# Kernel tuning notes

Measured on AMD Instinct MI355X. Metric: run time of the kernel, lower is better.

## Reference

```python
import jax, jax.numpy as jnp
import numpy as np

NUM_NODES = 100000
NUM_EDGES = 600000
NUM_GRAPHS = 1000
EMB = 128


def setup_inputs() -> dict:
    key = jax.random.key(0)
    ks = jax.random.split(key, 12)
    x = jax.random.normal(ks[0], (NUM_NODES, 4), dtype=jnp.float32)
    edge_index = jax.random.randint(ks[1], (2, NUM_EDGES), 0, NUM_NODES, dtype=jnp.int32)
    x_scalar = jax.random.normal(ks[2], (NUM_GRAPHS, 4), dtype=jnp.float32)
    batch_index = jnp.sort(jax.random.randint(ks[3], (NUM_NODES,), 0, NUM_GRAPHS, dtype=jnp.int32))
    def glorot(k, shape):
        fan_in, fan_out = shape[0], shape[1]
        s = jnp.sqrt(2.0 / (fan_in + fan_out)).astype(jnp.float32)
        return jax.random.normal(k, shape, dtype=jnp.float32) * s
    return {
        "x": x,
        "edge_index": edge_index,
        "x_scalar": x_scalar,
        "batch_index": batch_index,
        "W0": glorot(ks[4], (4, EMB)), "b0": jnp.zeros((EMB,), jnp.float32),
        "W1": glorot(ks[5], (EMB, EMB)), "b1": jnp.zeros((EMB,), jnp.float32),
        "W2": glorot(ks[6], (EMB, EMB)), "b2": jnp.zeros((EMB,), jnp.float32),
        "W3": glorot(ks[7], (EMB, EMB)), "b3": jnp.zeros((EMB,), jnp.float32),
        "Wl1": glorot(ks[8], (EMB + 4, 64)), "bl1": jnp.zeros((64,), jnp.float32),
        "Wl2": glorot(ks[9], (64, 1)), "bl2": jnp.zeros((1,), jnp.float32),
    }


def _gcn_norm(edge_index, num_nodes):
    # PyG GCNConv default: add self-loops, symmetric normalization
    loop = jnp.arange(num_nodes, dtype=edge_index.dtype)
    src = jnp.concatenate([edge_index[0], loop])
    dst = jnp.concatenate([edge_index[1], loop])
    deg = jax.ops.segment_sum(jnp.ones_like(src, dtype=jnp.float32), dst,
                              num_segments=num_nodes)
    dinv = jnp.where(deg > 0, jax.lax.rsqrt(jnp.maximum(deg, 1e-12)), 0.0)
    norm = dinv[src] * dinv[dst]  # [E+N]
    return src, dst, norm


def _gcn_conv(h, src, dst, norm, W, b, num_nodes):
    h = h @ W                                   # [N, out]
    msg = h[src] * norm[:, None]                # gather + normalize
    out = jax.ops.segment_sum(msg, dst, num_segments=num_nodes)  # scatter-add
    return out + b


def reference(x, edge_index, x_scalar, batch_index,
              W0, b0, W1, b1, W2, b2, W3, b3, Wl1, bl1, Wl2, bl2):
    n = x.shape[0]
    src, dst, norm = _gcn_norm(edge_index, n)
    h = jax.nn.relu(_gcn_conv(x, src, dst, norm, W0, b0, n))
    h = jax.nn.relu(_gcn_conv(h, src, dst, norm, W1, b1, n))
    h = jax.nn.relu(_gcn_conv(h, src, dst, norm, W2, b2, n))
    h = jax.nn.relu(_gcn_conv(h, src, dst, norm, W3, b3, n))
    # global mean pool over batch_index
    sums = jax.ops.segment_sum(h, batch_index, num_segments=NUM_GRAPHS)
    cnts = jax.ops.segment_sum(jnp.ones((n,), jnp.float32), batch_index,
                               num_segments=NUM_GRAPHS)
    pooled = sums / jnp.maximum(cnts, 1.0)[:, None]          # [G, EMB]
    feat = jnp.concatenate([pooled, x_scalar], axis=1)       # [G, EMB+4]
    out = jax.nn.relu(feat @ Wl1 + bl1) @ Wl2 + bl2          # [G, 1]
    return out
```

## Files before the change

kernel.cpp:

```cpp
#include <hip/hip_runtime.h>

#define NN 100000
#define EE 600000
#define GG 1000
#define NB ((NN + 255) / 256)
#define CAP 32
#define LDSPAD 136

typedef __bf16 bf16x8 __attribute__((ext_vector_type(8)));
typedef float f32x4 __attribute__((ext_vector_type(4)));
typedef unsigned int u32;

__device__ inline float2 bf2_to_f2(u32 u) {
  return make_float2(__uint_as_float(u << 16), __uint_as_float(u & 0xffff0000u));
}
__device__ inline u32 f2_to_bf2(float a, float b) {
  union { __bf16 h[2]; u32 u; } pk;
  pk.h[0] = (__bf16)a; pk.h[1] = (__bf16)b;
  return pk.u;
}


__global__ void k_init(int* cnt, int* gstart) {
  int i = blockIdx.x * 256 + threadIdx.x;
  if (i < NN) cnt[i] = 0;
  if (i <= GG) gstart[i] = NN;
}

__global__ void k_fill(const int* __restrict__ src, const int* __restrict__ dst,
                       int* cnt, int2* __restrict__ wbucket) {
  int e = blockIdx.x * 256 + threadIdx.x;
  if (e >= EE) return;
  int s = src[e], d = dst[e];
  int pos = atomicAdd(&cnt[d], 1);
  if (pos < CAP - 1) wbucket[d * CAP + pos].x = s;
}

__global__ void k_wb(const int* __restrict__ cnt, const int* __restrict__ batch,
                     int* gstart,
                     const float* __restrict__ W1, const float* __restrict__ W2,
                     const float* __restrict__ W3,
                     __bf16* __restrict__ Wt1, __bf16* __restrict__ Wt2,
                     __bf16* __restrict__ Wt3, int2* __restrict__ wbucket) {
  int gid = blockIdx.x * 256 + threadIdx.x;
  if (gid < 3 * 16384) {
    int which = gid >> 14, idx = gid & 16383;
    int n = idx >> 7, k = idx & 127;
    const float* W = (which == 0) ? W1 : (which == 1) ? W2 : W3;
    __bf16* Wt = (which == 0) ? Wt1 : (which == 1) ? Wt2 : Wt3;
    Wt[(size_t)n * 128 + k] = (__bf16)W[(size_t)k * 128 + n];
  }
  if (gid < NN) {
    int b = batch[gid];
    if (gid == 0) {
      for (int g = 0; g <= b; ++g) gstart[g] = 0;
    } else {
      int prev = batch[gid - 1];
      for (int g = prev + 1; g <= b; ++g) gstart[g] = gid;
    }
  }
  if (gid < NN * CAP) {
    int d = gid >> 5, slot = gid & 31;
    int m = min(cnt[d], CAP - 1);
    int mp = (m + 4) & ~3;
    if (slot < mp) {
      float dd = rsqrtf((float)(cnt[d] + 1));
      int s; float w;
      if (slot < m)      { s = wbucket[gid].x; w = rsqrtf((float)(cnt[s] + 1)) * dd; }
      else if (slot == m){ s = d;              w = dd * dd; }
      else               { s = d;              w = 0.f; }
      wbucket[gid] = make_int2(s, __float_as_int(w));
    }
  }
}

__global__ void k_l0(const float4* __restrict__ x, const int* __restrict__ cnt,
                     const int2* __restrict__ wbucket,
                     const float* __restrict__ W0, const float* __restrict__ b0,
                     u32* __restrict__ hout2) {
  int gid = blockIdx.x * 256 + threadIdx.x;
  if (gid >= NN * 16) return;
  int node = gid >> 4, cg = gid & 15;
  int m1 = min(cnt[node], CAP - 1) + 1;
  float4 yv = make_float4(0.f, 0.f, 0.f, 0.f);
  for (int e = 0; e < m1; ++e) {
    int2 md = wbucket[(size_t)node * CAP + e];
    float wgt = __int_as_float(md.y);
    float4 v = x[md.x];
    yv.x = fmaf(wgt, v.x, yv.x);
    yv.y = fmaf(wgt, v.y, yv.y);
    yv.z = fmaf(wgt, v.z, yv.z);
    yv.w = fmaf(wgt, v.w, yv.w);
  }
  float v[8];
  #pragma unroll
  for (int k = 0; k < 2; ++k) {
    float4 b = *(const float4*)(b0 + cg * 8 + k * 4);
    v[k * 4 + 0] = b.x; v[k * 4 + 1] = b.y; v[k * 4 + 2] = b.z; v[k * 4 + 3] = b.w;
  }
  #pragma unroll
  for (int k = 0; k < 4; ++k) {
    float yk = (k == 0) ? yv.x : (k == 1) ? yv.y : (k == 2) ? yv.z : yv.w;
    float4 wa = *(const float4*)(W0 + k * 128 + cg * 8);
    float4 wb = *(const float4*)(W0 + k * 128 + cg * 8 + 4);
    v[0] = fmaf(yk, wa.x, v[0]); v[1] = fmaf(yk, wa.y, v[1]);
    v[2] = fmaf(yk, wa.z, v[2]); v[3] = fmaf(yk, wa.w, v[3]);
    v[4] = fmaf(yk, wb.x, v[4]); v[5] = fmaf(yk, wb.y, v[5]);
    v[6] = fmaf(yk, wb.z, v[6]); v[7] = fmaf(yk, wb.w, v[7]);
  }
  uint4 o;
  o.x = f2_to_bf2(fmaxf(v[0], 0.f), fmaxf(v[1], 0.f));
  o.y = f2_to_bf2(fmaxf(v[2], 0.f), fmaxf(v[3], 0.f));
  o.z = f2_to_bf2(fmaxf(v[4], 0.f), fmaxf(v[5], 0.f));
  o.w = f2_to_bf2(fmaxf(v[6], 0.f), fmaxf(v[7], 0.f));
  *(uint4*)(hout2 + (size_t)node * 64 + cg * 4) = o;
}

__global__ __launch_bounds__(256) void k_agg23(const __bf16* __restrict__ hlin,
                                               const int* __restrict__ cnt,
                                               const int2* __restrict__ wbucket,
                                               u32* __restrict__ hout2) {
  int wid = (blockIdx.x * 4) + (threadIdx.x >> 6);
  int lane = threadIdx.x & 63;
  int ln = lane & 15, quad = lane >> 4;
  int na = wid * 2, nb = wid * 2 + 1;
  if (na >= NN) return;

  int mpa = (min(cnt[na], CAP - 1) + 4) & ~3;
  int mpb = (nb < NN) ? ((min(cnt[nb], CAP - 1) + 4) & ~3) : 0;
  int mpmin = min(mpa, mpb);

  int nodeL = (lane < 32) ? na : nb;
  int slot = lane & 31;
  int mymp = (lane < 32) ? mpa : mpb;
  int2 me = make_int2(0, 0);
  if (slot < mymp) me = wbucket[(size_t)nodeL * CAP + slot];
  int s_l = me.x, w_l = me.y;

  float aa[8] = {0.f, 0.f, 0.f, 0.f, 0.f, 0.f, 0.f, 0.f};
  float ab[8] = {0.f, 0.f, 0.f, 0.f, 0.f, 0.f, 0.f, 0.f};

  int j = 0;
  for (; j + 8 <= mpmin; j += 8) {
    int p0 = (j + quad) * 4, p1 = (j + 4 + quad) * 4;
    int sa0 = __builtin_amdgcn_ds_bpermute(p0, s_l);
    int sa1 = __builtin_amdgcn_ds_bpermute(p1, s_l);
    int sb0 = __builtin_amdgcn_ds_bpermute(128 + p0, s_l);
    int sb1 = __builtin_amdgcn_ds_bpermute(128 + p1, s_l);
    float wa0 = __int_as_float(__builtin_amdgcn_ds_bpermute(p0, w_l));
    float wa1 = __int_as_float(__builtin_amdgcn_ds_bpermute(p1, w_l));
    float wb0 = __int_as_float(__builtin_amdgcn_ds_bpermute(128 + p0, w_l));
    float wb1 = __int_as_float(__builtin_amdgcn_ds_bpermute(128 + p1, w_l));
    uint4 ua0 = *(const uint4*)(hlin + ((size_t)sa0 << 7) + ln * 8);
    uint4 ua1 = *(const uint4*)(hlin + ((size_t)sa1 << 7) + ln * 8);
    uint4 ub0 = *(const uint4*)(hlin + ((size_t)sb0 << 7) + ln * 8);
    uint4 ub1 = *(const uint4*)(hlin + ((size_t)sb1 << 7) + ln * 8);
    float2 f;
    f = bf2_to_f2(ua0.x); aa[0] = fmaf(wa0, f.x, aa[0]); aa[1] = fmaf(wa0, f.y, aa[1]);
    f = bf2_to_f2(ua0.y); aa[2] = fmaf(wa0, f.x, aa[2]); aa[3] = fmaf(wa0, f.y, aa[3]);
    f = bf2_to_f2(ua0.z); aa[4] = fmaf(wa0, f.x, aa[4]); aa[5] = fmaf(wa0, f.y, aa[5]);
    f = bf2_to_f2(ua0.w); aa[6] = fmaf(wa0, f.x, aa[6]); aa[7] = fmaf(wa0, f.y, aa[7]);
    f = bf2_to_f2(ua1.x); aa[0] = fmaf(wa1, f.x, aa[0]); aa[1] = fmaf(wa1, f.y, aa[1]);
    f = bf2_to_f2(ua1.y); aa[2] = fmaf(wa1, f.x, aa[2]); aa[3] = fmaf(wa1, f.y, aa[3]);
    f = bf2_to_f2(ua1.z); aa[4] = fmaf(wa1, f.x, aa[4]); aa[5] = fmaf(wa1, f.y, aa[5]);
    f = bf2_to_f2(ua1.w); aa[6] = fmaf(wa1, f.x, aa[6]); aa[7] = fmaf(wa1, f.y, aa[7]);
    f = bf2_to_f2(ub0.x); ab[0] = fmaf(wb0, f.x, ab[0]); ab[1] = fmaf(wb0, f.y, ab[1]);
    f = bf2_to_f2(ub0.y); ab[2] = fmaf(wb0, f.x, ab[2]); ab[3] = fmaf(wb0, f.y, ab[3]);
    f = bf2_to_f2(ub0.z); ab[4] = fmaf(wb0, f.x, ab[4]); ab[5] = fmaf(wb0, f.y, ab[5]);
    f = bf2_to_f2(ub0.w); ab[6] = fmaf(wb0, f.x, ab[6]); ab[7] = fmaf(wb0, f.y, ab[7]);
    f = bf2_to_f2(ub1.x); ab[0] = fmaf(wb1, f.x, ab[0]); ab[1] = fmaf(wb1, f.y, ab[1]);
    f = bf2_to_f2(ub1.y); ab[2] = fmaf(wb1, f.x, ab[2]); ab[3] = fmaf(wb1, f.y, ab[3]);
    f = bf2_to_f2(ub1.z); ab[4] = fmaf(wb1, f.x, ab[4]); ab[5] = fmaf(wb1, f.y, ab[5]);
    f = bf2_to_f2(ub1.w); ab[6] = fmaf(wb1, f.x, ab[6]); ab[7] = fmaf(wb1, f.y, ab[7]);
  }
  if (j < mpmin) {
    int p = (j + quad) * 4;
    int sa = __builtin_amdgcn_ds_bpermute(p, s_l);
    int sb = __builtin_amdgcn_ds_bpermute(128 + p, s_l);
    float wa = __int_as_float(__builtin_amdgcn_ds_bpermute(p, w_l));
    float wb = __int_as_float(__builtin_amdgcn_ds_bpermute(128 + p, w_l));
    uint4 ua = *(const uint4*)(hlin + ((size_t)sa << 7) + ln * 8);
    uint4 ub = *(const uint4*)(hlin + ((size_t)sb << 7) + ln * 8);
    float2 f;
    f = bf2_to_f2(ua.x); aa[0] = fmaf(wa, f.x, aa[0]); aa[1] = fmaf(wa, f.y, aa[1]);
    f = bf2_to_f2(ua.y); aa[2] = fmaf(wa, f.x, aa[2]); aa[3] = fmaf(wa, f.y, aa[3]);
    f = bf2_to_f2(ua.z); aa[4] = fmaf(wa, f.x, aa[4]); aa[5] = fmaf(wa, f.y, aa[5]);
    f = bf2_to_f2(ua.w); aa[6] = fmaf(wa, f.x, aa[6]); aa[7] = fmaf(wa, f.y, aa[7]);
    f = bf2_to_f2(ub.x); ab[0] = fmaf(wb, f.x, ab[0]); ab[1] = fmaf(wb, f.y, ab[1]);
    f = bf2_to_f2(ub.y); ab[2] = fmaf(wb, f.x, ab[2]); ab[3] = fmaf(wb, f.y, ab[3]);
    f = bf2_to_f2(ub.z); ab[4] = fmaf(wb, f.x, ab[4]); ab[5] = fmaf(wb, f.y, ab[5]);
    f = bf2_to_f2(ub.w); ab[6] = fmaf(wb, f.x, ab[6]); ab[7] = fmaf(wb, f.y, ab[7]);
    j += 4;
  }
  for (; j < mpa; j += 4) {
    int p = (j + quad) * 4;
    int s0 = __builtin_amdgcn_ds_bpermute(p, s_l);
    float w0 = __int_as_float(__builtin_amdgcn_ds_bpermute(p, w_l));
    uint4 u0 = *(const uint4*)(hlin + ((size_t)s0 << 7) + ln * 8);
    float2 f;
    f = bf2_to_f2(u0.x); aa[0] = fmaf(w0, f.x, aa[0]); aa[1] = fmaf(w0, f.y, aa[1]);
    f = bf2_to_f2(u0.y); aa[2] = fmaf(w0, f.x, aa[2]); aa[3] = fmaf(w0, f.y, aa[3]);
    f = bf2_to_f2(u0.z); aa[4] = fmaf(w0, f.x, aa[4]); aa[5] = fmaf(w0, f.y, aa[5]);
    f = bf2_to_f2(u0.w); aa[6] = fmaf(w0, f.x, aa[6]); aa[7] = fmaf(w0, f.y, aa[7]);
  }
  for (; j < mpb; j += 4) {
    int p = 128 + (j + quad) * 4;
    int s0 = __builtin_amdgcn_ds_bpermute(p, s_l);
    float w0 = __int_as_float(__builtin_amdgcn_ds_bpermute(p, w_l));
    uint4 u0 = *(const uint4*)(hlin + ((size_t)s0 << 7) + ln * 8);
    float2 f;
    f = bf2_to_f2(u0.x); ab[0] = fmaf(w0, f.x, ab[0]); ab[1] = fmaf(w0, f.y, ab[1]);
    f = bf2_to_f2(u0.y); ab[2] = fmaf(w0, f.x, ab[2]); ab[3] = fmaf(w0, f.y, ab[3]);
    f = bf2_to_f2(u0.z); ab[4] = fmaf(w0, f.x, ab[4]); ab[5] = fmaf(w0, f.y, ab[5]);
    f = bf2_to_f2(u0.w); ab[6] = fmaf(w0, f.x, ab[6]); ab[7] = fmaf(w0, f.y, ab[7]);
  }

  #pragma unroll
  for (int k = 0; k < 8; ++k) {
    aa[k] += __shfl_xor(aa[k], 16); aa[k] += __shfl_xor(aa[k], 32);
    ab[k] += __shfl_xor(ab[k], 16); ab[k] += __shfl_xor(ab[k], 32);
  }
  if (quad == 0) {
    uint4 oa;
    oa.x = f2_to_bf2(aa[0], aa[1]); oa.y = f2_to_bf2(aa[2], aa[3]);
    oa.z = f2_to_bf2(aa[4], aa[5]); oa.w = f2_to_bf2(aa[6], aa[7]);
    *(uint4*)(hout2 + (size_t)na * 64 + ln * 4) = oa;
    if (nb < NN) {
      uint4 ob;
      ob.x = f2_to_bf2(ab[0], ab[1]); ob.y = f2_to_bf2(ab[2], ab[3]);
      ob.z = f2_to_bf2(ab[4], ab[5]); ob.w = f2_to_bf2(ab[6], ab[7]);
      *(uint4*)(hout2 + (size_t)nb * 64 + ln * 4) = ob;
    }
  }
}

__global__ __launch_bounds__(256) void k_mfma(const __bf16* __restrict__ hin,
                                              const __bf16* __restrict__ Wt,
                                              const float* __restrict__ bias,
                                              __bf16* __restrict__ hout) {
  __shared__ __bf16 As[128 * LDSPAD];
  int tid = threadIdx.x;
  int row0 = blockIdx.x * 128;
  int lane = tid & 63, w = tid >> 6;
  int ln = lane & 15, quad = lane >> 4;

  bf16x8 bfrag[8][4];
  float bcol[8];
  #pragma unroll
  for (int nt = 0; nt < 8; ++nt) {
    bcol[nt] = bias[nt * 16 + ln];
    #pragma unroll
    for (int kc = 0; kc < 4; ++kc)
      bfrag[nt][kc] = *(const bf16x8*)(Wt + (size_t)(nt * 16 + ln) * 128 + kc * 32 + quad * 8);
  }

  #pragma unroll
  for (int i = 0; i < 8; ++i) {
    int eb = (i * 256 + tid) * 8;
    int r = eb >> 7, c = eb & 127;
    int gr = row0 + r;
    uint4 v = make_uint4(0, 0, 0, 0);
    if (gr < NN) v = *(const uint4*)(hin + (size_t)gr * 128 + c);
    *(uint4*)&As[r * LDSPAD + c] = v;
  }
  __syncthreads();

  f32x4 acc[2][8];
  #pragma unroll
  for (int rt = 0; rt < 2; ++rt)
    #pragma unroll
    for (int nt = 0; nt < 8; ++nt) acc[rt][nt] = (f32x4){0.f, 0.f, 0.f, 0.f};

  #pragma unroll
  for (int kc = 0; kc < 4; ++kc) {
    bf16x8 a0 = *(const bf16x8*)&As[(w * 32 + ln) * LDSPAD + kc * 32 + quad * 8];
    bf16x8 a1 = *(const bf16x8*)&As[(w * 32 + 16 + ln) * LDSPAD + kc * 32 + quad * 8];
    #pragma unroll
    for (int nt = 0; nt < 8; ++nt) {
      acc[0][nt] = __builtin_amdgcn_mfma_f32_16x16x32_bf16(a0, bfrag[nt][kc], acc[0][nt], 0, 0, 0);
      acc[1][nt] = __builtin_amdgcn_mfma_f32_16x16x32_bf16(a1, bfrag[nt][kc], acc[1][nt], 0, 0, 0);
    }
  }

  #pragma unroll
  for (int rt = 0; rt < 2; ++rt)
    #pragma unroll
    for (int nt = 0; nt < 8; ++nt)
      #pragma unroll
      for (int reg = 0; reg < 4; ++reg) {
        int gr = row0 + w * 32 + rt * 16 + quad * 4 + reg;
        if (gr < NN)
          hout[(size_t)gr * 128 + nt * 16 + ln] =
              (__bf16)fmaxf(acc[rt][nt][reg] + bcol[nt], 0.f);
      }
}

__global__ __launch_bounds__(256) void k_poolmlp(const uint2* __restrict__ h4u,
                                                 const int* __restrict__ gstart,
                                                 const float* __restrict__ xs,
                                                 const float* __restrict__ Wl1,
                                                 const float* __restrict__ bl1,
                                                 const float* __restrict__ Wl2,
                                                 const float* __restrict__ bl2,
                                                 float* __restrict__ out) {
  __shared__ float4 part[8][32];
  __shared__ float pooled[128];
  int g = blockIdx.x;
  int beg = gstart[g], end = gstart[g + 1];
  int tid = threadIdx.x;
  int cg = tid & 31;
  int rg = tid >> 5;
  float4 acc = make_float4(0.f, 0.f, 0.f, 0.f);
  for (int i = beg + rg; i < end; i += 8) {
    uint2 u = h4u[(size_t)i * 32 + cg];
    acc.x += __uint_as_float(u.x << 16);
    acc.y += __uint_as_float(u.x & 0xffff0000u);
    acc.z += __uint_as_float(u.y << 16);
    acc.w += __uint_as_float(u.y & 0xffff0000u);
  }
  part[rg][cg] = acc;
  __syncthreads();
  if (tid < 32) {
    float4 s = part[0][tid];
    #pragma unroll
    for (int r = 1; r < 8; ++r) {
      float4 v = part[r][tid];
      s.x += v.x; s.y += v.y; s.z += v.z; s.w += v.w;
    }
    float sc = 1.f / fmaxf((float)(end - beg), 1.f);
    pooled[tid * 4 + 0] = s.x * sc;
    pooled[tid * 4 + 1] = s.y * sc;
    pooled[tid * 4 + 2] = s.z * sc;
    pooled[tid * 4 + 3] = s.w * sc;
  }
  __syncthreads();
  if (tid < 64) {
    float hj = bl1[tid];
    #pragma unroll 4
    for (int k = 0; k < 128; ++k) hj = fmaf(pooled[k], Wl1[k * 64 + tid], hj);
    const float* xr = xs + g * 4;
    #pragma unroll
    for (int k = 0; k < 4; ++k) hj = fmaf(xr[k], Wl1[(128 + k) * 64 + tid], hj);
    hj = fmaxf(hj, 0.f);
    float val = hj * Wl2[tid];
    #pragma unroll
    for (int off = 32; off > 0; off >>= 1) val += __shfl_down(val, off);
    if (tid == 0) out[g] = val + bl2[0];
  }
}


extern "C" void kernel_launch(void* const* d_in, const int* in_sizes, int n_in,
                              void* d_out, int out_size, void* d_ws, size_t ws_size,
                              hipStream_t stream) {
  const float* x    = (const float*)d_in[0];
  const int*   ei   = (const int*)d_in[1];
  const float* xs   = (const float*)d_in[2];
  const int*   batch= (const int*)d_in[3];
  const float* W0   = (const float*)d_in[4];
  const float* b0   = (const float*)d_in[5];
  const float* W1   = (const float*)d_in[6];
  const float* b1   = (const float*)d_in[7];
  const float* W2   = (const float*)d_in[8];
  const float* b2   = (const float*)d_in[9];
  const float* W3   = (const float*)d_in[10];
  const float* b3   = (const float*)d_in[11];
  const float* Wl1  = (const float*)d_in[12];
  const float* bl1  = (const float*)d_in[13];
  const float* Wl2  = (const float*)d_in[14];
  const float* bl2  = (const float*)d_in[15];
  const int* srcA = ei;
  const int* dstA = ei + EE;
  float* out = (float*)d_out;

  char* p = (char*)d_ws;
  auto take = [&](size_t bytes) { char* q = p; p += (bytes + 255) & ~(size_t)255; return q; };
  __bf16* hA    = (__bf16*)take((size_t)NN * 128 * 2);
  __bf16* hB    = (__bf16*)take((size_t)NN * 128 * 2);
  int*    cnt   = (int*)take((size_t)NN * 4);
  int2*   wbucket = (int2*)take((size_t)NN * CAP * 8);
  int*    gstart= (int*)take((size_t)(GG + 1) * 4);
  __bf16* Wt1   = (__bf16*)take(16384 * 2);
  __bf16* Wt2   = (__bf16*)take(16384 * 2);
  __bf16* Wt3   = (__bf16*)take(16384 * 2);

  k_init<<<NB, 256, 0, stream>>>(cnt, gstart);
  k_fill<<<(EE + 255) / 256, 256, 0, stream>>>(srcA, dstA, cnt, wbucket);
  k_wb<<<(NN * CAP + 255) / 256, 256, 0, stream>>>(cnt, batch, gstart, W1, W2, W3,
                                                   Wt1, Wt2, Wt3, wbucket);

  k_l0<<<(NN * 16 + 255) / 256, 256, 0, stream>>>((const float4*)x, cnt, wbucket, W0, b0, (u32*)hA);
  k_agg23<<<(NN + 7) / 8, 256, 0, stream>>>(hA, cnt, wbucket, (u32*)hB);
  k_mfma<<<(NN + 127) / 128, 256, 0, stream>>>(hB, Wt1, b1, hA);
  k_agg23<<<(NN + 7) / 8, 256, 0, stream>>>(hA, cnt, wbucket, (u32*)hB);
  k_mfma<<<(NN + 127) / 128, 256, 0, stream>>>(hB, Wt2, b2, hA);
  k_agg23<<<(NN + 7) / 8, 256, 0, stream>>>(hA, cnt, wbucket, (u32*)hB);
  k_mfma<<<(NN + 127) / 128, 256, 0, stream>>>(hB, Wt3, b3, hA);

  k_poolmlp<<<GG, 256, 0, stream>>>((const uint2*)hA, gstart, xs, Wl1, bl1, Wl2, bl2, out);
}
```

Measured before the change: 349.9 us.

## Store aggregated features in MFMA fragment layout and drop LDS staging in k_mfma

The aggregation kernel now writes its output in a tiled layout of 16-node tiles that matches the MFMA operand fragment order. The GEMM kernel then loads fragments straight from global memory with no LDS staging or __syncthreads. It also swaps operand roles so each wave computes one 16-node tile and writes packed bf16 pairs per row. The aim is to remove LDS traffic and the barrier and to coalesce the input loads. The cost is reloading weight fragments from global or cache for every tile.

Result: slower. 380.2 us (+8.6%).

```diff
diff --git a/kernel.cpp b/kernel.cpp
--- a/kernel.cpp
+++ b/kernel.cpp
@@ -5,7 +5,7 @@
 #define GG 1000
 #define NB ((NN + 255) / 256)
 #define CAP 32
-#define LDSPAD 136
+#define NTILES (NN / 16)
 
 typedef __bf16 bf16x8 __attribute__((ext_vector_type(8)));
 typedef float f32x4 __attribute__((ext_vector_type(4)));
@@ -224,75 +224,51 @@
     uint4 oa;
     oa.x = f2_to_bf2(aa[0], aa[1]); oa.y = f2_to_bf2(aa[2], aa[3]);
     oa.z = f2_to_bf2(aa[4], aa[5]); oa.w = f2_to_bf2(aa[6], aa[7]);
-    *(uint4*)(hout2 + (size_t)na * 64 + ln * 4) = oa;
+    *(uint4*)(hout2 + (size_t)(na >> 4) * 1024 + ln * 64 + (na & 15) * 4) = oa;
     if (nb < NN) {
       uint4 ob;
       ob.x = f2_to_bf2(ab[0], ab[1]); ob.y = f2_to_bf2(ab[2], ab[3]);
       ob.z = f2_to_bf2(ab[4], ab[5]); ob.w = f2_to_bf2(ab[6], ab[7]);
-      *(uint4*)(hout2 + (size_t)nb * 64 + ln * 4) = ob;
-    }
-  }
-}
-
-__global__ __launch_bounds__(256) void k_mfma(const __bf16* __restrict__ hin,
+      *(uint4*)(hout2 + (size_t)(nb >> 4) * 1024 + ln * 64 + (nb & 15) * 4) = ob;
+    }
+  }
+}
+
+__global__ __launch_bounds__(256) void k_mfma(const __bf16* __restrict__ hfrag,
                                               const __bf16* __restrict__ Wt,
                                               const float* __restrict__ bias,
                                               __bf16* __restrict__ hout) {
-  __shared__ __bf16 As[128 * LDSPAD];
   int tid = threadIdx.x;
-  int row0 = blockIdx.x * 128;
   int lane = tid & 63, w = tid >> 6;
   int ln = lane & 15, quad = lane >> 4;
-
-  bf16x8 bfrag[8][4];
-  float bcol[8];
-  #pragma unroll
-  for (int nt = 0; nt < 8; ++nt) {
-    bcol[nt] = bias[nt * 16 + ln];
+  int tile = blockIdx.x * 4 + w;
+  if (tile >= NTILES) return;
+
+  f32x4 acc[8];
+  #pragma unroll
+  for (int ct = 0; ct < 8; ++ct) acc[ct] = (f32x4){0.f, 0.f, 0.f, 0.f};
+
+  const __bf16* hb = hfrag + (size_t)tile * 2048 + quad * 128 + ln * 8;
+  #pragma unroll
+  for (int kc = 0; kc < 4; ++kc) {
+    bf16x8 hf = *(const bf16x8*)(hb + kc * 512);
     #pragma unroll
-    for (int kc = 0; kc < 4; ++kc)
-      bfrag[nt][kc] = *(const bf16x8*)(Wt + (size_t)(nt * 16 + ln) * 128 + kc * 32 + quad * 8);
-  }
-
-  #pragma unroll
-  for (int i = 0; i < 8; ++i) {
-    int eb = (i * 256 + tid) * 8;
-    int r = eb >> 7, c = eb & 127;
-    int gr = row0 + r;
-    uint4 v = make_uint4(0, 0, 0, 0);
-    if (gr < NN) v = *(const uint4*)(hin + (size_t)gr * 128 + c);
-    *(uint4*)&As[r * LDSPAD + c] = v;
-  }
-  __syncthreads();
-
-  f32x4 acc[2][8];
-  #pragma unroll
-  for (int rt = 0; rt < 2; ++rt)
-    #pragma unroll
-    for (int nt = 0; nt < 8; ++nt) acc[rt][nt] = (f32x4){0.f, 0.f, 0.f, 0.f};
-
-  #pragma unroll
-  for (int kc = 0; kc < 4; ++kc) {
-    bf16x8 a0 = *(const bf16x8*)&As[(w * 32 + ln) * LDSPAD + kc * 32 + quad * 8];
-    bf16x8 a1 = *(const bf16x8*)&As[(w * 32 + 16 + ln) * LDSPAD + kc * 32 + quad * 8];
-    #pragma unroll
-    for (int nt = 0; nt < 8; ++nt) {
-      acc[0][nt] = __builtin_amdgcn_mfma_f32_16x16x32_bf16(a0, bfrag[nt][kc], acc[0][nt], 0, 0, 0);
-      acc[1][nt] = __builtin_amdgcn_mfma_f32_16x16x32_bf16(a1, bfrag[nt][kc], acc[1][nt], 0, 0, 0);
-    }
-  }
-
-  #pragma unroll
-  for (int rt = 0; rt < 2; ++rt)
-    #pragma unroll
-    for (int nt = 0; nt < 8; ++nt)
-      #pragma unroll
-      for (int reg = 0; reg < 4; ++reg) {
-        int gr = row0 + w * 32 + rt * 16 + quad * 4 + reg;
-        if (gr < NN)
-          hout[(size_t)gr * 128 + nt * 16 + ln] =
-              (__bf16)fmaxf(acc[rt][nt][reg] + bcol[nt], 0.f);
-      }
+    for (int ct = 0; ct < 8; ++ct) {
+      bf16x8 wf = *(const bf16x8*)(Wt + (size_t)(ct * 16 + ln) * 128 + kc * 32 + quad * 8);
+      acc[ct] = __builtin_amdgcn_mfma_f32_16x16x32_bf16(wf, hf, acc[ct], 0, 0, 0);
+    }
+  }
+
+  int node = tile * 16 + ln;
+  __bf16* op = hout + (size_t)node * 128 + quad * 4;
+  #pragma unroll
+  for (int ct = 0; ct < 8; ++ct) {
+    float4 bq = *(const float4*)(bias + ct * 16 + quad * 4);
+    uint2 o;
+    o.x = f2_to_bf2(fmaxf(acc[ct][0] + bq.x, 0.f), fmaxf(acc[ct][1] + bq.y, 0.f));
+    o.y = f2_to_bf2(fmaxf(acc[ct][2] + bq.z, 0.f), fmaxf(acc[ct][3] + bq.w, 0.f));
+    *(uint2*)(op + ct * 16) = o;
+  }
 }
 
 __global__ __launch_bounds__(256) void k_poolmlp(const uint2* __restrict__ h4u,
@@ -391,11 +367,11 @@
 
   k_l0<<<(NN * 16 + 255) / 256, 256, 0, stream>>>((const float4*)x, cnt, wbucket, W0, b0, (u32*)hA);
   k_agg23<<<(NN + 7) / 8, 256, 0, stream>>>(hA, cnt, wbucket, (u32*)hB);
-  k_mfma<<<(NN + 127) / 128, 256, 0, stream>>>(hB, Wt1, b1, hA);
+  k_mfma<<<(NTILES + 3) / 4, 256, 0, stream>>>(hB, Wt1, b1, hA);
   k_agg23<<<(NN + 7) / 8, 256, 0, stream>>>(hA, cnt, wbucket, (u32*)hB);
-  k_mfma<<<(NN + 127) / 128, 256, 0, stream>>>(hB, Wt2, b2, hA);
+  k_mfma<<<(NTILES + 3) / 4, 256, 0, stream>>>(hB, Wt2, b2, hA);
   k_agg23<<<(NN + 7) / 8, 256, 0, stream>>>(hA, cnt, wbucket, (u32*)hB);
-  k_mfma<<<(NN + 127) / 128, 256, 0, stream>>>(hB, Wt3, b3, hA);
+  k_mfma<<<(NTILES + 3) / 4, 256, 0, stream>>>(hB, Wt3, b3, hA);
 
   k_poolmlp<<<GG, 256, 0, stream>>>((const uint2*)hA, gstart, xs, Wl1, bl1, Wl2, bl2, out);
 }
```
